# Kernel optimization log

Hardware: AMD Instinct MI355X
Metric: run time of the kernel (lower is better)

The kernel has to match this reference:

```python
import jax, jax.numpy as jnp
import numpy as np

ID_THRESHOLD = 0.15   # args.id_threshod
SOFT_SCALE = 5.0      # args.soft_scale
K = 3                 # sorted_indices[1:4] -> up to 3 candidates per query


def setup_inputs() -> dict:
    key = jax.random.key(0)
    k1, k2, k3, k4 = jax.random.split(key, 4)
    B, N, D = 128, 200000, 512
    return {
        "i_feats": jax.random.normal(k1, (B, D), jnp.float32),
        "t_feats": jax.random.normal(k2, (B, D), jnp.float32),
        "img_memory": jax.random.normal(k3, (N, D), jnp.float32),
        "txt_memory": jax.random.normal(k4, (N, D), jnp.float32),
    }


def _l2norm(x):
    return x / jnp.linalg.norm(x, axis=-1, keepdims=True)


def reference(i_feats, t_feats, img_memory, txt_memory):
    B, D = i_feats.shape
    # dense cosine similarity vs. memory bank: [B, N]
    sim = _l2norm(i_feats) @ _l2norm(img_memory).T

    # top-(K+1) descending; drop the best match (self) like sorted_indices[1:4]
    vals, idx = jax.lax.top_k(sim, K + 1)
    cand_vals, cand_idx = vals[:, 1:], idx[:, 1:]          # [B, K]
    valid = cand_vals > ID_THRESHOLD                        # threshold gate

    # weight = (1 - softmax(soft_scale * [1.0, sims_valid]))[1:]
    neg_inf = jnp.float32(-1e30)
    logits = jnp.concatenate(
        [jnp.full((B, 1), SOFT_SCALE, sim.dtype),
         jnp.where(valid, SOFT_SCALE * cand_vals, neg_inf)], axis=1)  # [B, K+1]
    w = 1.0 - jax.nn.softmax(logits, axis=-1)
    sample_weight = jnp.where(valid, w[:, 1:], 0.0)         # [B, K]

    # gather positives from both memory banks; zero out padded (invalid) slots
    safe_idx = jnp.where(valid, cand_idx, 0)
    m = valid[..., None].astype(sim.dtype)
    pos_img = img_memory[safe_idx] * m                      # [B, K, D]
    pos_txt = txt_memory[safe_idx] * m

    new_img = jnp.concatenate([i_feats, pos_img.reshape(B * K, D)], 0)  # [B(1+K), D]
    new_txt = jnp.concatenate([t_feats, pos_txt.reshape(B * K, D)], 0)

    # pid label matrix: query i has pid i; its valid slots share pid i;
    # invalid (padded) slots get unique negative pids so they match only themselves
    qpid = jnp.arange(B)
    slot_global = jnp.arange(B * K).reshape(B, K)
    spid = jnp.where(valid, qpid[:, None], -(slot_global + 1))
    pid = jnp.concatenate([qpid, spid.reshape(-1)])          # [B(1+K)]
    labels = (pid[:, None] == pid[None, :]).astype(sim.dtype)

    # soften first-B rows: diagonal stays 1, matched memory slots get sample_weight
    soft_block = jnp.zeros((B, B, K), sim.dtype).at[qpid, qpid, :].set(sample_weight)
    top = jnp.concatenate([jnp.eye(B, dtype=sim.dtype), soft_block.reshape(B, B * K)], 1)
    labels = labels.at[:B, :].set(top)

    # single fused output: [2*B(1+K) + B(1+K), D]  (note B(1+K) == D here)
    return jnp.concatenate([new_img, new_txt, labels], axis=0)
```

## Files before the change

kernel.cpp:

```cpp
#include <hip/hip_runtime.h>
#include <hip/hip_bf16.h>
#include <math.h>

#define D      512
#define BQ     128
#define KK     3
#define THR    0.15f
#define SSCALE 5.0f
#define SENT   0x7fffffff
#define NBLK   256
#define NSTR   (NBLK * 4)
#define NB4    (NBLK * 4)
#define IDXM   0x3FFFFu

using bf16x8 = __attribute__((ext_vector_type(8))) short;
using f32x4  = __attribute__((ext_vector_type(4))) float;

__device__ __forceinline__ unsigned short f2bf(float x) {
    unsigned u = __float_as_uint(x);
    return (unsigned short)((u + 0x7fffu + ((u >> 16) & 1u)) >> 16);
}

__device__ __forceinline__ unsigned pk2(float lo, float hi) {
    __hip_bfloat162 h = __float22bfloat162_rn(make_float2(lo, hi));
    union { __hip_bfloat162 h; unsigned u; } c; c.h = h;
    return c.u;
}

__device__ __forceinline__ bf16x8 cvt8(float4 f0, float4 f1) {
    union { unsigned u[4]; bf16x8 v; } r;
    r.u[0] = pk2(f0.x, f0.y);
    r.u[1] = pk2(f0.z, f0.w);
    r.u[2] = pk2(f1.x, f1.y);
    r.u[3] = pk2(f1.z, f1.w);
    return r.v;
}

__device__ __forceinline__ unsigned ordf(float v) {
    unsigned u = __float_as_uint(v);
    return u ^ ((unsigned)((int)u >> 31) | 0x80000000u);
}

__device__ __forceinline__ void insk4(unsigned key, unsigned K[4]) {
    if (key > K[3]) {
        bool b0 = key > K[0], b1 = key > K[1], b2 = key > K[2];
        unsigned k0 = K[0], k1 = K[1], k2 = K[2];
        K[0] = b0 ? key : k0;
        K[1] = b0 ? k0 : (b1 ? key : k1);
        K[2] = b1 ? k1 : (b2 ? key : k2);
        K[3] = b2 ? k2 : key;
    }
}

__device__ __forceinline__ void insk8(unsigned key, unsigned* K) {
    if (key <= K[7]) return;
    #pragma unroll
    for (int k = 0; k < 8; ++k) {
        if (key > K[k]) {
            #pragma unroll
            for (int m = 7; m > k; --m) K[m] = K[m-1];
            K[k] = key;
            return;
        }
    }
}

template<int K>
__device__ __forceinline__ void insK(float v, int c, float* V, int* C) {
    #pragma unroll
    for (int k = 0; k < K; ++k) {
        if (v > V[k] || (v == V[k] && c < C[k])) {
            #pragma unroll
            for (int m = K - 1; m > k; --m) { V[m] = V[m-1]; C[m] = C[m-1]; }
            V[k] = v; C[k] = c;
            return;
        }
    }
}

__global__ void prep_kernel(const float* __restrict__ x, float* __restrict__ ihat,
                            uint4* __restrict__ apre) {
    int r = blockIdx.x;
    int l = threadIdx.x;
    const float4* row = (const float4*)(x + (size_t)r * D);
    float4 v0 = row[l * 2 + 0];
    float4 v1 = row[l * 2 + 1];
    float s = v0.x*v0.x + v0.y*v0.y + v0.z*v0.z + v0.w*v0.w
            + v1.x*v1.x + v1.y*v1.y + v1.z*v1.z + v1.w*v1.w;
    #pragma unroll
    for (int off = 32; off > 0; off >>= 1) s += __shfl_xor(s, off);
    float inv = 1.0f / sqrtf(s);
    float a0 = v0.x*inv, a1 = v0.y*inv, a2 = v0.z*inv, a3 = v0.w*inv;
    float a4 = v1.x*inv, a5 = v1.y*inv, a6 = v1.z*inv, a7 = v1.w*inv;
    float4* orow = (float4*)(ihat + (size_t)r * D);
    orow[l*2+0] = make_float4(a0, a1, a2, a3);
    orow[l*2+1] = make_float4(a4, a5, a6, a7);
    uint4 p;
    p.x = f2bf(a0) | ((unsigned)f2bf(a1) << 16);
    p.y = f2bf(a2) | ((unsigned)f2bf(a3) << 16);
    p.z = f2bf(a4) | ((unsigned)f2bf(a5) << 16);
    p.w = f2bf(a6) | ((unsigned)f2bf(a7) << 16);
    apre[((l & 3) << 11) + ((l >> 2) << 7) + r] = p;
}

__global__ __launch_bounds__(512)
void sim_topk(const uint4* __restrict__ apre, const float* __restrict__ img,
              int N, int ntiles, int nit, unsigned* __restrict__ pk)
{
    extern __shared__ __align__(16) unsigned char Bs[];
    const int tid  = threadIdx.x;
    const int lane = tid & 63;
    const int wid  = tid >> 6;
    const int lr   = lane & 15;
    const int kg   = lane >> 4;
    const int h    = wid & 1;
    const int pr   = wid >> 1;

    #pragma unroll
    for (int j = 0; j < 16; ++j) {
        int s = tid + j * 512;
        uint4 p = apre[s];
        int addr = ((s >> 7) & 15) * 8192 + (s >> 11) * 2048 + (s & 127) * 16;
        *(uint4*)(Bs + addr) = p;
    }
    __syncthreads();

    const int lane_off = kg * 2048 + h * 1024 + lr * 16;

    unsigned keys[4][4];
    #pragma unroll
    for (int nf = 0; nf < 4; ++nf)
        #pragma unroll
        for (int s = 0; s < 4; ++s) keys[nf][s] = 0u;

    const int sid = blockIdx.x * 4 + pr;
    int t = sid;
    const float* gp;
    {
        int row = t * 16 + lr;
        if (row >= N) row = N - 1;
        gp = img + (size_t)row * D + kg * 8;
    }

    float4 pre[4][2];
    if (t < ntiles) {
        #pragma unroll
        for (int c = 0; c < 4; ++c) {
            pre[c][0] = *(const float4*)(gp + c * 32);
            pre[c][1] = *(const float4*)(gp + c * 32 + 4);
        }
    }

#define CHUNK(c) do {                                                          \
        float4 f0_ = pre[(c) & 3][0], f1_ = pre[(c) & 3][1];                   \
        if ((c) < 12) {                                                        \
            pre[(c) & 3][0] = *(const float4*)(gp + ((c) + 4) * 32);           \
            pre[(c) & 3][1] = *(const float4*)(gp + ((c) + 4) * 32 + 4);       \
        } else {                                                               \
            pre[(c) & 3][0] = *(const float4*)(gpn + ((c) - 12) * 32);         \
            pre[(c) & 3][1] = *(const float4*)(gpn + ((c) - 12) * 32 + 4);     \
        }                                                                      \
        sq += f0_.x*f0_.x + f0_.y*f0_.y + f0_.z*f0_.z + f0_.w*f0_.w            \
            + f1_.x*f1_.x + f1_.y*f1_.y + f1_.z*f1_.z + f1_.w*f1_.w;           \
        bf16x8 a_ = cvt8(f0_, f1_);                                            \
        const unsigned char* bp_ = Bs + (c) * 8192 + lane_off;                 \
        _Pragma("unroll")                                                      \
        for (int nf_ = 0; nf_ < 4; ++nf_) {                                    \
            bf16x8 b_ = *(const bf16x8*)(bp_ + nf_ * 256);                     \
            acc[nf_] = __builtin_amdgcn_mfma_f32_16x16x32_bf16(a_, b_, acc[nf_], 0, 0, 0); \
        }                                                                      \
    } while (0)

    for (int it = 0; it < nit; ++it) {
        int tn = t + NSTR;
        if (t < ntiles) {
            const float* gpn;
            {
                int tt = (tn < ntiles) ? tn : t;
                int row = tt * 16 + lr;
                if (row >= N) row = N - 1;
                gpn = img + (size_t)row * D + kg * 8;
            }
            f32x4 acc[4];
            #pragma unroll
            for (int nf = 0; nf < 4; ++nf) acc[nf] = (f32x4){0.f, 0.f, 0.f, 0.f};
            float sq = 0.f;

            CHUNK(0);  CHUNK(1);  CHUNK(2);  CHUNK(3);
            CHUNK(4);  CHUNK(5);  CHUNK(6);  CHUNK(7);
            CHUNK(8);  CHUNK(9);  CHUNK(10); CHUNK(11);
            CHUNK(12); CHUNK(13); CHUNK(14); CHUNK(15);

            float s2 = sq;
            s2 += __shfl_xor(s2, 16);
            s2 += __shfl_xor(s2, 32);
            float rnorm = s2 > 0.f ? rsqrtf(s2) : 0.f;

            const int ib = t * 16 + kg * 4;
            #pragma unroll
            for (int g = 0; g < 4; ++g) {
                int idx = ib + g;
                bool ok = idx < N;
                unsigned ic = (unsigned)idx ^ IDXM;
                float r = __shfl(rnorm, kg * 4 + g);
                #pragma unroll
                for (int nf = 0; nf < 4; ++nf) {
                    unsigned o   = ordf(acc[nf][g] * r);
                    unsigned key = ok ? ((o & 0xFFFC0000u) | ic) : 0u;
                    insk4(key, keys[nf]);
                }
            }
            gp = gpn;
        }
        t = tn;
        __builtin_amdgcn_s_barrier();
    }
#undef CHUNK

    #pragma unroll
    for (int nf = 0; nf < 4; ++nf) {
        #pragma unroll
        for (int st = 0; st < 2; ++st) {
            const int off = st ? 32 : 16;
            unsigned mk[4];
            #pragma unroll
            for (int s = 0; s < 4; ++s) mk[s] = __shfl_xor((int)keys[nf][s], off);
            #pragma unroll
            for (int s = 0; s < 4; ++s) insk4(mk[s], keys[nf]);
        }
    }

    __syncthreads();
    if (kg == 0) {
        #pragma unroll
        for (int nf = 0; nf < 4; ++nf) {
            int q = h * 64 + nf * 16 + lr;
            uint4 v;
            v.x = keys[nf][0]; v.y = keys[nf][1]; v.z = keys[nf][2]; v.w = keys[nf][3];
            *(uint4*)(Bs + ((size_t)pr * 128 + q) * 16) = v;
        }
    }
    __syncthreads();
    if (tid < BQ) {
        int q = tid;
        unsigned V[4] = {0u, 0u, 0u, 0u};
        #pragma unroll
        for (int w = 0; w < 4; ++w) {
            uint4 kk = *(const uint4*)(Bs + ((size_t)w * 128 + q) * 16);
            insk4(kk.x, V); insk4(kk.y, V); insk4(kk.z, V); insk4(kk.w, V);
        }
        uint4 o; o.x = V[0]; o.y = V[1]; o.z = V[2]; o.w = V[3];
        *(uint4*)(pk + (size_t)q * NB4 + (size_t)blockIdx.x * 4) = o;
    }
}

__global__ __launch_bounds__(256)
void reduce_rescore(const unsigned* __restrict__ pk, int nb4,
                    const float* __restrict__ ihat, const float* __restrict__ img, int N,
                    float* __restrict__ swo, int* __restrict__ sidxo,
                    int* __restrict__ valido)
{
    __shared__ unsigned lk[256][8];
    __shared__ float sv[8];
    __shared__ int   si[8];
    const int r = blockIdx.x, tid = threadIdx.x;

    unsigned K[8];
    #pragma unroll
    for (int k = 0; k < 8; ++k) K[k] = 0u;
    const unsigned* prow = pk + (size_t)r * nb4;
    for (int j = tid; j < nb4; j += 256) insk8(prow[j], K);
    #pragma unroll
    for (int k = 0; k < 8; ++k) lk[tid][k] = K[k];
    __syncthreads();
    if (tid < 16) {
        for (int o = 1; o < 16; ++o) {
            int t2 = tid + o * 16;
            #pragma unroll
            for (int s = 0; s < 8; ++s) insk8(lk[t2][s], K);
        }
        #pragma unroll
        for (int k = 0; k < 8; ++k) lk[tid][k] = K[k];
    }
    __syncthreads();
    if (tid == 0) {
        for (int o = 1; o < 16; ++o)
            #pragma unroll
            for (int s = 0; s < 8; ++s) insk8(lk[o][s], K);
        #pragma unroll
        for (int k = 0; k < 8; ++k) {
            int idx = (int)((K[k] & IDXM) ^ IDXM);
            si[k] = (K[k] != 0u && idx < N) ? idx : -1;
        }
    }
    __syncthreads();

    {
        const int k = tid >> 5, l = tid & 31;
        int idx = si[k];
        float dot = 0.f, ssq = 0.f;
        if (idx >= 0) {
            const float* a = ihat + (size_t)r * D + l * 16;
            const float* b = img + (size_t)idx * D + l * 16;
            #pragma unroll
            for (int j = 0; j < 4; ++j) {
                float4 va = *(const float4*)(a + j*4);
                float4 vb = *(const float4*)(b + j*4);
                dot += va.x*vb.x + va.y*vb.y + va.z*vb.z + va.w*vb.w;
                ssq += vb.x*vb.x + vb.y*vb.y + vb.z*vb.z + vb.w*vb.w;
            }
        }
        #pragma unroll
        for (int o = 16; o > 0; o >>= 1) { dot += __shfl_xor(dot, o); ssq += __shfl_xor(ssq, o); }
        if (l == 0) sv[k] = (idx >= 0 && ssq > 0.f) ? dot * rsqrtf(ssq) : -1e30f;
    }
    __syncthreads();

    if (tid == 0) {
        float Vt[4]; int Ct[4];
        #pragma unroll
        for (int k = 0; k < 4; ++k) { Vt[k] = -1e30f; Ct[k] = SENT; }
        #pragma unroll
        for (int k = 0; k < 8; ++k)
            if (si[k] >= 0) insK<4>(sv[k], si[k], Vt, Ct);
        float lg[4]; int vd[3];
        lg[0] = SSCALE;
        #pragma unroll
        for (int k = 0; k < 3; ++k) {
            vd[k] = (Vt[k+1] > THR) ? 1 : 0;
            lg[k+1] = vd[k] ? SSCALE * Vt[k+1] : -1e30f;
        }
        float m = fmaxf(fmaxf(lg[0], lg[1]), fmaxf(lg[2], lg[3]));
        float e0 = expf(lg[0]-m), e1 = expf(lg[1]-m), e2 = expf(lg[2]-m), e3 = expf(lg[3]-m);
        float sum = e0 + e1 + e2 + e3;
        float ee[3] = {e1, e2, e3};
        #pragma unroll
        for (int k = 0; k < 3; ++k) {
            float w = 1.0f - ee[k] / sum;
            swo[r*3+k]    = vd[k] ? w : 0.0f;
            sidxo[r*3+k]  = vd[k] ? Ct[k+1] : 0;
            valido[r*3+k] = vd[k];
        }
    }
}

__global__ void assemble_kernel(const float* __restrict__ i_feats, const float* __restrict__ t_feats,
                                const float* __restrict__ img, const float* __restrict__ txt,
                                const float* __restrict__ sw, const int* __restrict__ sidx,
                                const int* __restrict__ valid, float* __restrict__ out)
{
    const int r = blockIdx.x;
    const int t = threadIdx.x;
    float4* orow = (float4*)(out + (size_t)r * D);
    if (r < 128) {
        orow[t] = ((const float4*)(i_feats + (size_t)r * D))[t];
    } else if (r < 512) {
        int s = r - 128;
        float4 v = make_float4(0.f,0.f,0.f,0.f);
        if (valid[s]) v = ((const float4*)(img + (size_t)sidx[s] * D))[t];
        orow[t] = v;
    } else if (r < 640) {
        orow[t] = ((const float4*)(t_feats + (size_t)(r - 512) * D))[t];
    } else if (r < 1024) {
        int s = r - 640;
        float4 v = make_float4(0.f,0.f,0.f,0.f);
        if (valid[s]) v = ((const float4*)(txt + (size_t)sidx[s] * D))[t];
        orow[t] = v;
    } else {
        int li = r - 1024;
        float o[4];
        int j0 = t * 4;
        if (li < 128) {
            #pragma unroll
            for (int u = 0; u < 4; ++u) {
                int j = j0 + u;
                if (j < 128) o[u] = (j == li) ? 1.0f : 0.0f;
                else {
                    int s = j - 128;
                    o[u] = (s / 3 == li) ? sw[li*3 + (s % 3)] : 0.0f;
                }
            }
        } else {
            int i2 = li - 128;
            int b = i2 / 3;
            int vi = valid[i2];
            #pragma unroll
            for (int u = 0; u < 4; ++u) {
                int j = j0 + u;
                float val;
                if (j < 128) val = (vi && j == b) ? 1.0f : 0.0f;
                else {
                    int s2 = j - 128;
                    int vj = valid[s2];
                    int b2 = s2 / 3;
                    if (vi && vj)        val = (b == b2) ? 1.0f : 0.0f;
                    else if (!vi && !vj) val = (i2 == s2) ? 1.0f : 0.0f;
                    else                 val = 0.0f;
                }
                o[u] = val;
            }
        }
        orow[t] = make_float4(o[0], o[1], o[2], o[3]);
    }
}

extern "C" void kernel_launch(void* const* d_in, const int* in_sizes, int n_in,
                              void* d_out, int out_size, void* d_ws, size_t ws_size,
                              hipStream_t stream) {
    const float* i_feats = (const float*)d_in[0];
    const float* t_feats = (const float*)d_in[1];
    const float* img     = (const float*)d_in[2];
    const float* txt     = (const float*)d_in[3];
    float* out = (float*)d_out;

    const int N      = in_sizes[2] / D;
    const int ntiles = (N + 15) / 16;
    const int nit    = (ntiles + NSTR - 1) / NSTR;

    char* ws = (char*)d_ws;
    size_t off = 0;
    float*    ihat = (float*)(ws + off);    off += (size_t)BQ * D * 4;
    uint4*    apre = (uint4*)(ws + off);    off += (size_t)BQ * D * 2;
    unsigned* pk   = (unsigned*)(ws + off); off += (size_t)BQ * NB4 * 4;
    float*    swv  = (float*)(ws + off);    off += BQ * 4 * 4;
    int*      sidx = (int*)(ws + off);      off += BQ * 4 * 4;
    int*      vld  = (int*)(ws + off);      off += BQ * 4 * 4;

    prep_kernel<<<BQ, 64, 0, stream>>>(i_feats, ihat, apre);
    sim_topk<<<NBLK, 512, 131072, stream>>>(apre, img, N, ntiles, nit, pk);
    reduce_rescore<<<BQ, 256, 0, stream>>>(pk, NB4, ihat, img, N, swv, sidx, vld);
    assemble_kernel<<<3 * (BQ + BQ * KK), 128, 0, stream>>>(i_feats, t_feats, img, txt,
                                                            swv, sidx, vld, out);
}
```

Measured before the change: 206.4 us.

## Split sim_topk queries across two block halves to halve LDS and raise occupancy

The similarity/top-k kernel now launches twice as many blocks. Each block holds only 64 of the 128 query vectors in a static 64KB LDS buffer, and each of its 8 waves streams its own memory-bank tile instead of pairs of waves sharing a tile. The per-iteration workgroup barrier is also removed. The aim is more resident waves per CU and less synchronisation. The cost is that every memory-bank row is now fetched by two separate blocks, which relies on L2/MALL hits to avoid doubling global traffic.

```diff
diff --git a/kernel.cpp b/kernel.cpp
--- a/kernel.cpp
+++ b/kernel.cpp
@@ -9,7 +9,7 @@
 #define SSCALE 5.0f
 #define SENT   0x7fffffff
 #define NBLK   256
-#define NSTR   (NBLK * 4)
+#define NSTR   (NBLK * 8)
 #define NB4    (NBLK * 4)
 #define IDXM   0x3FFFFu
 
@@ -107,25 +107,25 @@
 void sim_topk(const uint4* __restrict__ apre, const float* __restrict__ img,
               int N, int ntiles, int nit, unsigned* __restrict__ pk)
 {
-    extern __shared__ __align__(16) unsigned char Bs[];
+    __shared__ __align__(16) unsigned char Bs[65536];
     const int tid  = threadIdx.x;
     const int lane = tid & 63;
     const int wid  = tid >> 6;
     const int lr   = lane & 15;
     const int kg   = lane >> 4;
-    const int h    = wid & 1;
-    const int pr   = wid >> 1;
-
-    #pragma unroll
-    for (int j = 0; j < 16; ++j) {
+    const int qh   = blockIdx.x >> 8;
+    const int tg   = blockIdx.x & 255;
+
+    #pragma unroll
+    for (int j = 0; j < 8; ++j) {
         int s = tid + j * 512;
-        uint4 p = apre[s];
-        int addr = ((s >> 7) & 15) * 8192 + (s >> 11) * 2048 + (s & 127) * 16;
-        *(uint4*)(Bs + addr) = p;
-    }
-    __syncthreads();
-
-    const int lane_off = kg * 2048 + h * 1024 + lr * 16;
+        int q_ = s & 63, c = (s >> 6) & 15, g = s >> 10;
+        uint4 p = apre[g * 2048 + c * 128 + qh * 64 + q_];
+        *(uint4*)(Bs + c * 4096 + g * 1024 + q_ * 16) = p;
+    }
+    __syncthreads();
+
+    const int lane_off = kg * 1024 + lr * 16;
 
     unsigned keys[4][4];
     #pragma unroll
@@ -133,8 +133,7 @@
         #pragma unroll
         for (int s = 0; s < 4; ++s) keys[nf][s] = 0u;
 
-    const int sid = blockIdx.x * 4 + pr;
-    int t = sid;
+    int t = tg * 8 + wid;
     const float* gp;
     {
         int row = t * 16 + lr;
@@ -163,7 +162,7 @@
         sq += f0_.x*f0_.x + f0_.y*f0_.y + f0_.z*f0_.z + f0_.w*f0_.w            \
             + f1_.x*f1_.x + f1_.y*f1_.y + f1_.z*f1_.z + f1_.w*f1_.w;           \
         bf16x8 a_ = cvt8(f0_, f1_);                                            \
-        const unsigned char* bp_ = Bs + (c) * 8192 + lane_off;                 \
+        const unsigned char* bp_ = Bs + (c) * 4096 + lane_off;                 \
         _Pragma("unroll")                                                      \
         for (int nf_ = 0; nf_ < 4; ++nf_) {                                    \
             bf16x8 b_ = *(const bf16x8*)(bp_ + nf_ * 256);                     \
@@ -213,7 +212,6 @@
             gp = gpn;
         }
         t = tn;
-        __builtin_amdgcn_s_barrier();
     }
 #undef CHUNK
 
@@ -234,23 +232,24 @@
     if (kg == 0) {
         #pragma unroll
         for (int nf = 0; nf < 4; ++nf) {
-            int q = h * 64 + nf * 16 + lr;
+            int q_ = nf * 16 + lr;
             uint4 v;
             v.x = keys[nf][0]; v.y = keys[nf][1]; v.z = keys[nf][2]; v.w = keys[nf][3];
-            *(uint4*)(Bs + ((size_t)pr * 128 + q) * 16) = v;
-        }
-    }
-    __syncthreads();
-    if (tid < BQ) {
-        int q = tid;
+            *(uint4*)(Bs + ((size_t)wid * 64 + q_) * 16) = v;
+        }
+    }
+    __syncthreads();
+    if (tid < 64) {
+        int q_ = tid;
         unsigned V[4] = {0u, 0u, 0u, 0u};
         #pragma unroll
-        for (int w = 0; w < 4; ++w) {
-            uint4 kk = *(const uint4*)(Bs + ((size_t)w * 128 + q) * 16);
+        for (int w = 0; w < 8; ++w) {
+            uint4 kk = *(const uint4*)(Bs + ((size_t)w * 64 + q_) * 16);
             insk4(kk.x, V); insk4(kk.y, V); insk4(kk.z, V); insk4(kk.w, V);
         }
+        int q = qh * 64 + q_;
         uint4 o; o.x = V[0]; o.y = V[1]; o.z = V[2]; o.w = V[3];
-        *(uint4*)(pk + (size_t)q * NB4 + (size_t)blockIdx.x * 4) = o;
+        *(uint4*)(pk + (size_t)q * NB4 + (size_t)tg * 4) = o;
     }
 }
 
@@ -427,7 +426,7 @@
     int*      vld  = (int*)(ws + off);      off += BQ * 4 * 4;
 
     prep_kernel<<<BQ, 64, 0, stream>>>(i_feats, ihat, apre);
-    sim_topk<<<NBLK, 512, 131072, stream>>>(apre, img, N, ntiles, nit, pk);
+    sim_topk<<<2 * NBLK, 512, 0, stream>>>(apre, img, N, ntiles, nit, pk);
     reduce_rescore<<<BQ, 256, 0, stream>>>(pk, NB4, ihat, img, N, swv, sidx, vld);
     assemble_kernel<<<3 * (BQ + BQ * KK), 128, 0, stream>>>(i_feats, t_feats, img, txt,
                                                             swv, sidx, vld, out);
```

Measured after the change: 243.3 us. 17.9% more time.
